# Kernel tuning notes

Hardware: AMD Instinct MI355X
Metric: run time of the kernel (lower is better)

Reference implementation:

```python
import jax, jax.numpy as jnp
import numpy as np

N = 20000      # num nodes
E = 320000     # num edges (avg degree 16)
R = 8          # num relations
D = 256        # input_dim / hidden dim
L = 6          # num_layers
EE = 32        # edge_embed_dim
B = 64         # batch size
K = 32         # num_negative + 1


def _layer_norm(x, g, b, eps=1e-5):
    mu = jnp.mean(x, axis=-1, keepdims=True)
    var = jnp.var(x, axis=-1, keepdims=True)
    return (x - mu) * jax.lax.rsqrt(var + eps) * g + b


def setup_inputs() -> dict:
    key = jax.random.key(0)
    ks = jax.random.split(key, 10)
    edge_index = jax.random.randint(ks[0], (2, E), 0, N)
    edge_type = jax.random.randint(ks[1], (E,), 0, R)
    edge_embed = jax.random.normal(ks[2], (E, EE), dtype=jnp.float32)
    src = jax.random.randint(ks[3], (B, K), 0, N)
    tgt = jax.random.randint(ks[4], (B, K), 0, N)
    rel = jax.random.randint(ks[5], (B, K), 0, R)
    batch = jnp.stack([src, tgt, rel], axis=-1)  # [B, K, 3]
    s = 1.0 / np.sqrt(D)
    W = jax.random.normal(ks[6], (L, R, D, D), dtype=jnp.float32) * s      # per-relation weights
    Wself = jax.random.normal(ks[7], (L, D, D), dtype=jnp.float32) * s     # self-loop weights
    We = jax.random.normal(ks[8], (L, EE, D), dtype=jnp.float32) * (1.0 / np.sqrt(EE))  # edge-embed proj (stage add)
    gamma = jnp.ones((L, D), dtype=jnp.float32)
    beta = jnp.zeros((L, D), dtype=jnp.float32)
    rel_emb = jax.random.normal(ks[9], (R, D), dtype=jnp.float32) * s      # DistMult relation embedding
    return dict(edge_index=edge_index, edge_type=edge_type, edge_embed=edge_embed,
                batch=batch, W=W, Wself=Wself, We=We, gamma=gamma, beta=beta,
                rel_emb=rel_emb)


def reference(edge_index, edge_type, edge_embed, batch, W, Wself, We, gamma, beta, rel_emb):
    src, dst = edge_index[0], edge_index[1]
    # mean aggregation denominator: in-degree per node (over all relations)
    deg = jnp.clip(jax.ops.segment_sum(jnp.ones((E,), jnp.float32), dst, num_segments=N), 1.0)
    # segment id combining relation and destination node -> aggregate-then-transform trick
    seg = edge_type * N + dst
    x = jnp.ones((N, D), dtype=jnp.float32)
    for l in range(L):
        # stage 'add': message = x[src] + proj(edge_embed)
        msg = x[src] + edge_embed @ We[l]                                  # [E, D]
        agg = jax.ops.segment_sum(msg, seg, num_segments=R * N).reshape(R, N, D)
        h = jnp.einsum('rnd,rdf->nf', agg, W[l]) / deg[:, None] + x @ Wself[l]
        h = jax.nn.relu(_layer_norm(h, gamma[l], beta[l]))
        x = h + x  # short_cut residual
    # DistMult scoring: gather source/target/relation embeddings, mul, sum
    s_emb = x[batch[..., 0]]          # [B, K, D]
    t_emb = x[batch[..., 1]]          # [B, K, D]
    r_emb = rel_emb[batch[..., 2]]    # [B, K, D]
    return jnp.sum(s_emb * r_emb * t_emb, axis=-1)  # [B, K]
```

## Files before the change

kernel.cpp:

```cpp
#include <hip/hip_runtime.h>
#include <hip/hip_bf16.h>

#define NN 20000
#define NP 20080
#define NE 320000
#define RR 8
#define DD 256
#define LL 6
#define EED 32
#define BB 64
#define KK 32
#define MM (NN * RR)
#define NSB 79
#define BMR 80
#define NGB 251
#define YROW 2304
#define YROWB 4608

typedef __bf16 bf8 __attribute__((ext_vector_type(8)));
typedef float f4 __attribute__((ext_vector_type(4)));

__device__ inline float lo2f(unsigned v) { return __uint_as_float(v << 16); }
__device__ inline float hi2f(unsigned v) { return __uint_as_float(v & 0xffff0000u); }
__device__ inline unsigned short f2bf(float f) {
    unsigned u = __float_as_uint(f);
    return (unsigned short)((u + 0x7fff + ((u >> 16) & 1)) >> 16);
}
__device__ inline unsigned pack2(float lo, float hi) {
    return (unsigned)f2bf(lo) | ((unsigned)f2bf(hi) << 16);
}

#define GLOAD_LDS16(src, dst)                                                  \
    __builtin_amdgcn_global_load_lds(                                          \
        (const __attribute__((address_space(1))) unsigned int*)(src),          \
        (__attribute__((address_space(3))) unsigned int*)(dst), 16, 0, 0)


__global__ __launch_bounds__(256) void hist_kernel(const int* __restrict__ dstv,
                                                   const int* __restrict__ typev,
                                                   int* __restrict__ hist) {
    int e = blockIdx.x * 256 + threadIdx.x;
    if (e < NE) atomicAdd(&hist[dstv[e] * 8 + typev[e]], 1);
}

__global__ __launch_bounds__(256) void scan1_kernel(const int* __restrict__ hist,
                                                    int* __restrict__ excl,
                                                    int* __restrict__ bsums) {
    __shared__ int tmp[256];
    int tid = threadIdx.x;
    int base = blockIdx.x * 2048 + tid * 8;
    int v[8]; int s = 0;
#pragma unroll
    for (int i = 0; i < 8; ++i) {
        v[i] = (base + i < MM) ? hist[base + i] : 0;
        s += v[i];
    }
    tmp[tid] = s;
    __syncthreads();
    for (int off = 1; off < 256; off <<= 1) {
        int t = (tid >= off) ? tmp[tid - off] : 0;
        __syncthreads();
        tmp[tid] += t;
        __syncthreads();
    }
    int run = tmp[tid] - s;
#pragma unroll
    for (int i = 0; i < 8; ++i) {
        if (base + i < MM) excl[base + i] = run;
        run += v[i];
    }
    if (tid == 255) bsums[blockIdx.x] = tmp[255];
}

__global__ __launch_bounds__(128) void scan2_kernel(int* __restrict__ bsums) {
    __shared__ int tmp[128];
    int tid = threadIdx.x;
    int orig = (tid < NSB) ? bsums[tid] : 0;
    tmp[tid] = orig;
    __syncthreads();
    for (int off = 1; off < 128; off <<= 1) {
        int t = (tid >= off) ? tmp[tid - off] : 0;
        __syncthreads();
        tmp[tid] += t;
        __syncthreads();
    }
    if (tid < NSB) bsums[tid] = tmp[tid] - orig;
}

__global__ __launch_bounds__(256) void add_off_kernel(const int* __restrict__ excl,
                                                      const int* __restrict__ bsums,
                                                      int* __restrict__ seg_start,
                                                      int* __restrict__ cursor) {
    int i = blockIdx.x * 256 + threadIdx.x;
    if (i < MM) {
        int v = excl[i] + bsums[i >> 11];
        seg_start[i] = v;
        cursor[i] = v;
    }
    if (i == 0) seg_start[MM] = NE;
}

__global__ __launch_bounds__(256) void sort_scatter_kernel(
    const int* __restrict__ srcv, const int* __restrict__ dstv,
    const int* __restrict__ typev, int* __restrict__ cursor,
    int* __restrict__ esrcY, int* __restrict__ eid) {
    int e = blockIdx.x * 256 + threadIdx.x;
    if (e < NE) {
        int key = dstv[e] * 8 + typev[e];
        int pos = atomicAdd(&cursor[key], 1);
        esrcY[pos] = srcv[e] * YROWB + typev[e] * 512;
        eid[pos]   = e;
    }
}

__global__ __launch_bounds__(256) void invdeg_kernel(const int* __restrict__ seg_start,
                                                     float* __restrict__ invdeg) {
    int i = blockIdx.x * 256 + threadIdx.x;
    if (i < NN) {
        int d = seg_start[i * 8 + 8] - seg_start[i * 8];
        invdeg[i] = 1.0f / (float)max(d, 1);
    }
}


__global__ __launch_bounds__(256) void eagg_kernel(
    const int* __restrict__ seg_start, const int* __restrict__ eid,
    const float* __restrict__ ee, const float* __restrict__ invdeg,
    unsigned short* __restrict__ eaggbf) {
    int tid = threadIdx.x;
    int s = blockIdx.x * 8 + (tid >> 5);
    int j = tid & 31;
    int n = s >> 3, r = s & 7;
    int j0 = seg_start[s], j1 = seg_start[s + 1];
    float sum = 0.0f;
    for (int p = j0; p < j1; ++p)
        sum += ee[eid[p] * EED + j];
    eaggbf[(size_t)n * DD + r * EED + j] = f2bf(sum * invdeg[n]);
}

__global__ __launch_bounds__(256) void whe_kernel(const float* __restrict__ We,
                                                  const float* __restrict__ W,
                                                  float* __restrict__ Whe) {
    __shared__ float WeS[EED * 32];
    int b = blockIdx.x;
    int l = b >> 6;
    int r = (b >> 3) & 7;
    int dc = b & 7;
    int tid = threadIdx.x;
    {
        int j = tid >> 3, dl = (tid & 7) * 4;
        *(float4*)&WeS[j * 32 + dl] =
            *(const float4*)&We[(size_t)l * EED * DD + (size_t)j * DD + dc * 32 + dl];
    }
    __syncthreads();
    const float* Wr = W + ((size_t)l * 8 + r) * DD * DD + (size_t)dc * 32 * DD;
    float acc[EED];
#pragma unroll
    for (int j = 0; j < EED; ++j) acc[j] = 0.0f;
    for (int dl = 0; dl < 32; ++dl) {
        float w = Wr[(size_t)dl * DD + tid];
#pragma unroll
        for (int j = 0; j < EED; ++j) acc[j] += WeS[j * 32 + dl] * w;
    }
    float* outp = Whe + (size_t)l * DD * DD + r * EED * DD + tid;
#pragma unroll
    for (int j = 0; j < EED; ++j) unsafeAtomicAdd(&outp[j * DD], acc[j]);
}

__global__ __launch_bounds__(256) void bswz_kernel(const float* __restrict__ W,
                                                   const float* __restrict__ Wself,
                                                   const float* __restrict__ Whe,
                                                   unsigned short* __restrict__ Bsw) {
    int gid = blockIdx.x * 256 + threadIdx.x;
    int f = gid & 255;
    int t = gid >> 8;
    int quad = t & 3; t >>= 2;
    int kb = t & 7; t >>= 3;
    int p = t % 10, l = t / 10;
    const float* base = (p <= 7) ? W + ((size_t)l * 8 + p) * DD * DD
                      : (p == 8) ? Wself + (size_t)l * DD * DD
                                 : Whe + (size_t)l * DD * DD;
    int k0 = kb * 32 + quad * 8;
    unsigned pk[4];
#pragma unroll
    for (int jj = 0; jj < 4; ++jj)
        pk[jj] = pack2(base[(size_t)(k0 + 2 * jj) * DD + f],
                       base[(size_t)(k0 + 2 * jj + 1) * DD + f]);
    uint4 v = make_uint4(pk[0], pk[1], pk[2], pk[3]);
    *(uint4*)&Bsw[(size_t)gid * 8] = v;
}

__global__ __launch_bounds__(256) void init_x_kernel(float* __restrict__ xA,
                                                     float* __restrict__ xB,
                                                     unsigned short* __restrict__ xbfA,
                                                     unsigned short* __restrict__ xbfB) {
    int i = blockIdx.x * 256 + threadIdx.x;
    ((float4*)xA)[i] = make_float4(1.f, 1.f, 1.f, 1.f);
    ((float4*)xB)[i] = make_float4(1.f, 1.f, 1.f, 1.f);
    ((uint2*)xbfA)[i] = make_uint2(0x3f803f80u, 0x3f803f80u);
    ((uint2*)xbfB)[i] = make_uint2(0x3f803f80u, 0x3f803f80u);
}

__global__ __launch_bounds__(512) void ymm_kernel(
    const unsigned short* __restrict__ Asrc, const unsigned short* __restrict__ Bswl,
    unsigned short* __restrict__ Yout, int rtBeg, int rtEnd, int ostride) {
    __shared__ __align__(16) unsigned char smem[40960 + 81920];
    unsigned char* As = smem;
    float* Hs = (float*)(smem + 40960);
    int tid = threadIdx.x;
    int wv = tid >> 6, lane = tid & 63;
    int row0 = blockIdx.x * BMR;
    int m = lane & 15, quad = lane >> 4;

#pragma unroll
    for (int i = 0; i < 5; ++i) {
        int bc = i * 512 + wv * 64;
        int c = bc + lane;
        int row = c >> 5, sc = c & 31, scs = sc ^ (row & 31);
        GLOAD_LDS16(Asrc + (size_t)(row0 + row) * DD + scs * 8, As + (size_t)c * 16);
    }
    int gn0 = rtBeg * 8, gnEnd = rtEnd * 8;
    bf8 breg[2][2];
#pragma unroll
    for (int nt = 0; nt < 2; ++nt) {
        breg[0][nt] = *(const bf8*)&Bswl[(((size_t)gn0 * 4 + quad) * 256 + wv * 32 + nt * 16 + m) * 8];
        breg[1][nt] = *(const bf8*)&Bswl[(((size_t)(gn0 + 1) * 4 + quad) * 256 + wv * 32 + nt * 16 + m) * 8];
    }
    __syncthreads();

#pragma unroll 1
    for (int rt = rtBeg; rt < rtEnd; ++rt) {
        f4 acc[5][2] = {};
#pragma unroll
        for (int kb = 0; kb < 8; ++kb) {
            bf8 afr[5];
#pragma unroll
            for (int mt = 0; mt < 5; ++mt) {
                int rowl = mt * 16 + m;
                afr[mt] = *(bf8*)&As[rowl * 512 + (((kb * 4 + quad) ^ (rowl & 31)) * 16)];
            }
#pragma unroll
            for (int mt = 0; mt < 5; ++mt)
#pragma unroll
                for (int nt = 0; nt < 2; ++nt)
                    acc[mt][nt] = __builtin_amdgcn_mfma_f32_16x16x32_bf16(
                        afr[mt], breg[kb & 1][nt], acc[mt][nt], 0, 0, 0);
            int gn = rt * 8 + kb + 2;
            if (gn < gnEnd) {
#pragma unroll
                for (int nt = 0; nt < 2; ++nt)
                    breg[kb & 1][nt] = *(const bf8*)&Bswl[((size_t)gn * 4 + quad) * 2048
                                                          + ((size_t)(wv * 32 + nt * 16 + m)) * 8];
            }
        }
#pragma unroll
        for (int mt = 0; mt < 5; ++mt)
#pragma unroll
            for (int nt = 0; nt < 2; ++nt)
#pragma unroll
                for (int rg = 0; rg < 4; ++rg)
                    Hs[(mt * 16 + quad * 4 + rg) * 256 + wv * 32 + nt * 16 + m] = acc[mt][nt][rg];
        __syncthreads();
        int colOff = (rt - rtBeg) * 256;
#pragma unroll
        for (int c2 = 0; c2 < 10; ++c2) {
            int li = c2 * 512 + tid;
            int row = li >> 6, u4 = li & 63;
            float4 v = *(float4*)&Hs[row * 256 + u4 * 4];
            *(uint2*)&Yout[(size_t)(row0 + row) * ostride + colOff + u4 * 4] =
                make_uint2(pack2(v.x, v.y), pack2(v.z, v.w));
        }
        __syncthreads();
    }
}

__global__ __launch_bounds__(512) void aggln_kernel(
    const int* __restrict__ seg_start, const int* __restrict__ esrcY,
    const unsigned short* __restrict__ Y, const unsigned short* __restrict__ eterml,
    const float* __restrict__ xin, const float* __restrict__ gl,
    const float* __restrict__ bl, float* __restrict__ xout,
    unsigned short* __restrict__ xbfout) {
    int tid = threadIdx.x;
    int wv = tid >> 6, lane = tid & 63;
    int n = blockIdx.x * 8 + wv;
    float4 g  = *(const float4*)&gl[lane * 4];
    float4 bb = *(const float4*)&bl[lane * 4];
    int j0 = seg_start[n * 8], j1 = seg_start[n * 8 + 8];
    float idg = 1.0f / (float)max(j1 - j0, 1);
    const char* Yb = (const char*)Y;
    size_t lo8 = (size_t)(lane * 8);
    float a0 = 0.f, a1 = 0.f, a2 = 0.f, a3 = 0.f;
#pragma unroll 1
    for (int j = j0; j < j1; j += 8) {
        int rem = j1 - j;
        uint2 gvv[8];
#pragma unroll
        for (int t = 0; t < 8; ++t) {
            int jj = (t < rem) ? j + t : j;
            gvv[t] = *(const uint2*)(Yb + (size_t)(unsigned)esrcY[jj] + lo8);
        }
#pragma unroll
        for (int t = 0; t < 8; ++t) {
            unsigned vx = (t < rem) ? gvv[t].x : 0u;
            unsigned vy = (t < rem) ? gvv[t].y : 0u;
            a0 += lo2f(vx); a1 += hi2f(vx);
            a2 += lo2f(vy); a3 += hi2f(vy);
        }
    }
    uint2 sv = *(const uint2*)(Yb + (size_t)n * YROWB + 4096 + lo8);
    uint2 ev = *(const uint2*)&eterml[(size_t)n * DD + lane * 4];
    float h0 = a0 * idg + lo2f(sv.x) + lo2f(ev.x);
    float h1 = a1 * idg + hi2f(sv.x) + hi2f(ev.x);
    float h2 = a2 * idg + lo2f(sv.y) + lo2f(ev.y);
    float h3 = a3 * idg + hi2f(sv.y) + hi2f(ev.y);
    float s = h0 + h1 + h2 + h3;
    float q = h0 * h0 + h1 * h1 + h2 * h2 + h3 * h3;
#pragma unroll
    for (int off = 32; off; off >>= 1) {
        s += __shfl_xor(s, off);
        q += __shfl_xor(q, off);
    }
    float mu  = s * (1.0f / DD);
    float var = q * (1.0f / DD) - mu * mu;
    float rs  = rsqrtf(var + 1e-5f);
    size_t xi = (size_t)n * DD + lane * 4;
    float4 xv = *(const float4*)&xin[xi];
    float4 o;
    o.x = fmaxf((h0 - mu) * rs * g.x + bb.x, 0.0f) + xv.x;
    o.y = fmaxf((h1 - mu) * rs * g.y + bb.y, 0.0f) + xv.y;
    o.z = fmaxf((h2 - mu) * rs * g.z + bb.z, 0.0f) + xv.z;
    o.w = fmaxf((h3 - mu) * rs * g.w + bb.w, 0.0f) + xv.w;
    *(float4*)&xout[xi] = o;
    *(uint2*)&xbfout[xi] = make_uint2(pack2(o.x, o.y), pack2(o.z, o.w));
}

__global__ __launch_bounds__(256) void score_kernel(
    const int* __restrict__ batch, const float* __restrict__ x,
    const float* __restrict__ rel_emb, float* __restrict__ out) {
    int tid = threadIdx.x;
    int wave = tid >> 6, lane = tid & 63;
    int idx = blockIdx.x * 4 + wave;
    int s = batch[idx * 3 + 0], t = batch[idx * 3 + 1], r = batch[idx * 3 + 2];
    float4 sv = *(const float4*)&x[(size_t)s * DD + lane * 4];
    float4 tv = *(const float4*)&x[(size_t)t * DD + lane * 4];
    float4 rv = *(const float4*)&rel_emb[(size_t)r * DD + lane * 4];
    float sum = sv.x * rv.x * tv.x + sv.y * rv.y * tv.y +
                sv.z * rv.z * tv.z + sv.w * rv.w * tv.w;
#pragma unroll
    for (int off = 32; off; off >>= 1) sum += __shfl_xor(sum, off);
    if (lane == 0) out[idx] = sum;
}

extern "C" void kernel_launch(void* const* d_in, const int* in_sizes, int n_in,
                              void* d_out, int out_size, void* d_ws, size_t ws_size,
                              hipStream_t stream) {
    const int*   edge_index = (const int*)d_in[0];
    const int*   srcv   = edge_index;
    const int*   dstv   = edge_index + NE;
    const int*   typev  = (const int*)d_in[1];
    const float* ee     = (const float*)d_in[2];
    const int*   batch  = (const int*)d_in[3];
    const float* W      = (const float*)d_in[4];
    const float* Wself  = (const float*)d_in[5];
    const float* We     = (const float*)d_in[6];
    const float* gamma  = (const float*)d_in[7];
    const float* beta   = (const float*)d_in[8];
    const float* rel_emb= (const float*)d_in[9];
    float* out = (float*)d_out;

    float* xA     = (float*)d_ws;
    float* xB     = xA + (size_t)NP * DD;
    float* Whe    = xB + (size_t)NP * DD;
    float* invdeg = Whe + (size_t)LL * DD * DD;
    unsigned short* xbfA   = (unsigned short*)(invdeg + NN);
    unsigned short* xbfB   = xbfA + (size_t)NP * DD;
    unsigned short* eaggbf = xbfB + (size_t)NP * DD;
    unsigned short* Bsw    = eaggbf + (size_t)NP * DD;
    int* hist      = (int*)(Bsw + (size_t)LL * 2560 * DD);
    int* excl      = hist + MM;
    int* seg_start = excl + MM;
    int* cursor    = seg_start + MM + 1;
    int* bsums     = cursor + MM;
    int* esrcY     = bsums + 256;
    int* eid       = esrcY + NE;
    unsigned short* etermb =
        (unsigned short*)(((uintptr_t)(eid + NE) + 255) & ~(uintptr_t)255);
    unsigned short* Y = etermb + (size_t)NP * DD;

    hipMemsetAsync(hist, 0, MM * sizeof(int), stream);
    hist_kernel<<<(NE + 255) / 256, 256, 0, stream>>>(dstv, typev, hist);
    scan1_kernel<<<NSB, 256, 0, stream>>>(hist, excl, bsums);
    scan2_kernel<<<1, 128, 0, stream>>>(bsums);
    add_off_kernel<<<(MM + 255) / 256, 256, 0, stream>>>(excl, bsums, seg_start, cursor);
    invdeg_kernel<<<(NN + 255) / 256, 256, 0, stream>>>(seg_start, invdeg);
    sort_scatter_kernel<<<(NE + 255) / 256, 256, 0, stream>>>(srcv, dstv, typev, cursor, esrcY, eid);

    eagg_kernel<<<MM / 8, 256, 0, stream>>>(seg_start, eid, ee, invdeg, eaggbf);
    hipMemsetAsync(Whe, 0, (size_t)LL * DD * DD * sizeof(float), stream);
    whe_kernel<<<LL * 64, 256, 0, stream>>>(We, W, Whe);
    bswz_kernel<<<LL * 10 * 8 * 4, 256, 0, stream>>>(W, Wself, Whe, Bsw);
    init_x_kernel<<<(NP * DD / 4) / 256, 256, 0, stream>>>(xA, xB, xbfA, xbfB);

    float* xin = xA;  float* xout = xB;
    unsigned short* xbin = xbfA;  unsigned short* xbout = xbfB;
    for (int l = 0; l < LL; ++l) {
        const unsigned short* Bl = Bsw + (size_t)l * 2560 * DD;
        ymm_kernel<<<NGB, 512, 0, stream>>>(xbin, Bl, Y, 0, 9, YROW);
        ymm_kernel<<<NGB, 512, 0, stream>>>(eaggbf, Bl, etermb, 9, 10, DD);
        aggln_kernel<<<NN / 8, 512, 0, stream>>>(seg_start, esrcY, Y, etermb,
            xin, gamma + (size_t)l * DD, beta + (size_t)l * DD, xout, xbout);
        float* t = xin; xin = xout; xout = t;
        unsigned short* tb = xbin; xbin = xbout; xbout = tb;
    }
    score_kernel<<<(BB * KK) / 4, 256, 0, stream>>>(batch, xin, rel_emb, out);
}
```

Before: 755.6 us.

## Fuse per-layer GEMM launches and deepen gather unrolling in aggregation kernels

Measured after the change: 779.5 us. 1.03x slower.

```diff
diff --git a/kernel.cpp b/kernel.cpp
--- a/kernel.cpp
+++ b/kernel.cpp
@@ -133,8 +133,21 @@
     int n = s >> 3, r = s & 7;
     int j0 = seg_start[s], j1 = seg_start[s + 1];
     float sum = 0.0f;
-    for (int p = j0; p < j1; ++p)
-        sum += ee[eid[p] * EED + j];
+#pragma unroll 1
+    for (int p = j0; p < j1; p += 4) {
+        int rem = j1 - p;
+        int e4[4];
+        float fv[4];
+#pragma unroll
+        for (int t = 0; t < 4; ++t)
+            e4[t] = eid[(t < rem) ? p + t : p];
+#pragma unroll
+        for (int t = 0; t < 4; ++t)
+            fv[t] = ee[(size_t)e4[t] * EED + j];
+#pragma unroll
+        for (int t = 0; t < 4; ++t)
+            sum += (t < rem) ? fv[t] : 0.0f;
+    }
     eaggbf[(size_t)n * DD + r * EED + j] = f2bf(sum * invdeg[n]);
 }
 
@@ -202,8 +215,9 @@
 }
 
 __global__ __launch_bounds__(512) void ymm_kernel(
-    const unsigned short* __restrict__ Asrc, const unsigned short* __restrict__ Bswl,
-    unsigned short* __restrict__ Yout, int rtBeg, int rtEnd, int ostride) {
+    const unsigned short* __restrict__ xbfin, const unsigned short* __restrict__ eaggbf,
+    const unsigned short* __restrict__ Bswl, unsigned short* __restrict__ Y,
+    unsigned short* __restrict__ etermb) {
     __shared__ __align__(16) unsigned char smem[40960 + 81920];
     unsigned char* As = smem;
     float* Hs = (float*)(smem + 40960);
@@ -217,19 +231,29 @@
         int bc = i * 512 + wv * 64;
         int c = bc + lane;
         int row = c >> 5, sc = c & 31, scs = sc ^ (row & 31);
-        GLOAD_LDS16(Asrc + (size_t)(row0 + row) * DD + scs * 8, As + (size_t)c * 16);
-    }
-    int gn0 = rtBeg * 8, gnEnd = rtEnd * 8;
+        GLOAD_LDS16(xbfin + (size_t)(row0 + row) * DD + scs * 8, As + (size_t)c * 16);
+    }
     bf8 breg[2][2];
 #pragma unroll
     for (int nt = 0; nt < 2; ++nt) {
-        breg[0][nt] = *(const bf8*)&Bswl[(((size_t)gn0 * 4 + quad) * 256 + wv * 32 + nt * 16 + m) * 8];
-        breg[1][nt] = *(const bf8*)&Bswl[(((size_t)(gn0 + 1) * 4 + quad) * 256 + wv * 32 + nt * 16 + m) * 8];
+        breg[0][nt] = *(const bf8*)&Bswl[((size_t)quad * 256 + wv * 32 + nt * 16 + m) * 8];
+        breg[1][nt] = *(const bf8*)&Bswl[(((size_t)4 + quad) * 256 + wv * 32 + nt * 16 + m) * 8];
     }
     __syncthreads();
 
 #pragma unroll 1
-    for (int rt = rtBeg; rt < rtEnd; ++rt) {
+    for (int rt = 0; rt < 10; ++rt) {
+        if (rt == 9) {
+            __syncthreads();
+#pragma unroll
+            for (int i = 0; i < 5; ++i) {
+                int bc = i * 512 + wv * 64;
+                int c = bc + lane;
+                int row = c >> 5, sc = c & 31, scs = sc ^ (row & 31);
+                GLOAD_LDS16(eaggbf + (size_t)(row0 + row) * DD + scs * 8, As + (size_t)c * 16);
+            }
+            __syncthreads();
+        }
         f4 acc[5][2] = {};
 #pragma unroll
         for (int kb = 0; kb < 8; ++kb) {
@@ -246,13 +270,14 @@
                     acc[mt][nt] = __builtin_amdgcn_mfma_f32_16x16x32_bf16(
                         afr[mt], breg[kb & 1][nt], acc[mt][nt], 0, 0, 0);
             int gn = rt * 8 + kb + 2;
-            if (gn < gnEnd) {
+            if (gn < 80) {
 #pragma unroll
                 for (int nt = 0; nt < 2; ++nt)
                     breg[kb & 1][nt] = *(const bf8*)&Bswl[((size_t)gn * 4 + quad) * 2048
                                                           + ((size_t)(wv * 32 + nt * 16 + m)) * 8];
             }
         }
+        if (rt > 0) __syncthreads();
 #pragma unroll
         for (int mt = 0; mt < 5; ++mt)
 #pragma unroll
@@ -261,16 +286,17 @@
                 for (int rg = 0; rg < 4; ++rg)
                     Hs[(mt * 16 + quad * 4 + rg) * 256 + wv * 32 + nt * 16 + m] = acc[mt][nt][rg];
         __syncthreads();
-        int colOff = (rt - rtBeg) * 256;
+        unsigned short* outb = (rt < 9) ? Y : etermb;
+        size_t ostride = (rt < 9) ? YROW : DD;
+        int colOff = (rt < 9) ? rt * 256 : 0;
 #pragma unroll
         for (int c2 = 0; c2 < 10; ++c2) {
             int li = c2 * 512 + tid;
             int row = li >> 6, u4 = li & 63;
             float4 v = *(float4*)&Hs[row * 256 + u4 * 4];
-            *(uint2*)&Yout[(size_t)(row0 + row) * ostride + colOff + u4 * 4] =
+            *(uint2*)&outb[(size_t)(row0 + row) * ostride + colOff + u4 * 4] =
                 make_uint2(pack2(v.x, v.y), pack2(v.z, v.w));
         }
-        __syncthreads();
     }
 }
 
@@ -291,16 +317,16 @@
     size_t lo8 = (size_t)(lane * 8);
     float a0 = 0.f, a1 = 0.f, a2 = 0.f, a3 = 0.f;
 #pragma unroll 1
-    for (int j = j0; j < j1; j += 8) {
+    for (int j = j0; j < j1; j += 16) {
         int rem = j1 - j;
-        uint2 gvv[8];
-#pragma unroll
-        for (int t = 0; t < 8; ++t) {
+        uint2 gvv[16];
+#pragma unroll
+        for (int t = 0; t < 16; ++t) {
             int jj = (t < rem) ? j + t : j;
             gvv[t] = *(const uint2*)(Yb + (size_t)(unsigned)esrcY[jj] + lo8);
         }
 #pragma unroll
-        for (int t = 0; t < 8; ++t) {
+        for (int t = 0; t < 16; ++t) {
             unsigned vx = (t < rem) ? gvv[t].x : 0u;
             unsigned vy = (t < rem) ? gvv[t].y : 0u;
             a0 += lo2f(vx); a1 += hi2f(vx);
@@ -405,8 +431,7 @@
     unsigned short* xbin = xbfA;  unsigned short* xbout = xbfB;
     for (int l = 0; l < LL; ++l) {
         const unsigned short* Bl = Bsw + (size_t)l * 2560 * DD;
-        ymm_kernel<<<NGB, 512, 0, stream>>>(xbin, Bl, Y, 0, 9, YROW);
-        ymm_kernel<<<NGB, 512, 0, stream>>>(eaggbf, Bl, etermb, 9, 10, DD);
+        ymm_kernel<<<NGB, 512, 0, stream>>>(xbin, eaggbf, Bl, Y, etermb);
         aggln_kernel<<<NN / 8, 512, 0, stream>>>(seg_start, esrcY, Y, etermb,
             xin, gamma + (size_t)l * DD, beta + (size_t)l * DD, xout, xbout);
         float* t = xin; xin = xout; xout = t;
```
